# Optimization experiments

Hardware: AMD Instinct MI355X
Metric: run time of the kernel (lower is better)

## Reference

```python
import jax, jax.numpy as jnp
import numpy as np

H = 256   # hidden size
U = 10    # attention units


def _lstm_cell(xt, h, c, Wih, Whh, bih, bhh):
    # PyTorch gate order: i, f, g, o
    gates = xt @ Wih.T + h @ Whh.T + bih + bhh          # [B, 4H]
    i, f, g, o = jnp.split(gates, 4, axis=-1)
    i = jax.nn.sigmoid(i); f = jax.nn.sigmoid(f)
    g = jnp.tanh(g);       o = jax.nn.sigmoid(o)
    c = f * c + i * g
    h = o * jnp.tanh(c)
    return h, c


def setup_inputs() -> dict:
    key = jax.random.key(0)
    ks = jax.random.split(key, 12)
    B, S = 512, 256
    s = 1.0 / np.sqrt(H)
    x = jax.random.normal(ks[0], (B, S), dtype=jnp.float32)
    y = jax.random.randint(ks[1], (B, S), 0, S, dtype=jnp.int64)
    return {
        "x": x,
        "y": y,
        "enc_Wih": jax.random.uniform(ks[2], (4 * H, 1), jnp.float32, -s, s),
        "enc_Whh": jax.random.uniform(ks[3], (4 * H, H), jnp.float32, -s, s),
        "enc_bih": jax.random.uniform(ks[4], (4 * H,), jnp.float32, -s, s),
        "enc_bhh": jax.random.uniform(ks[5], (4 * H,), jnp.float32, -s, s),
        "dec_Wih": jax.random.uniform(ks[6], (4 * H, H + 1), jnp.float32, -s, s),
        "dec_Whh": jax.random.uniform(ks[7], (4 * H, H), jnp.float32, -s, s),
        "dec_bih": jax.random.uniform(ks[8], (4 * H,), jnp.float32, -s, s),
        "dec_bhh": jax.random.uniform(ks[9], (4 * H,), jnp.float32, -s, s),
        "att_W1": jax.random.uniform(ks[10], (U, H), jnp.float32, -s, s),
        "att_W2": jax.random.uniform(ks[11], (U, H), jnp.float32, -s, s),
        "att_V": jax.random.uniform(jax.random.fold_in(key, 99), (1, U), jnp.float32, -s, s),
    }


def reference(x, y, enc_Wih, enc_Whh, enc_bih, enc_bhh,
              dec_Wih, dec_Whh, dec_bih, dec_bhh,
              att_W1, att_W2, att_V):
    B, S = x.shape

    # ---- Encoder: LSTM over sequence of scalar inputs ----
    def enc_step(carry, xt):  # xt: [B, 1]
        h, c = carry
        h, c = _lstm_cell(xt, h, c, enc_Wih, enc_Whh, enc_bih, enc_bhh)
        return (h, c), h

    h0 = jnp.zeros((B, H), x.dtype)
    (hN, cN), enc_out_t = jax.lax.scan(enc_step, (h0, h0), x.T[:, :, None])
    enc_out = jnp.transpose(enc_out_t, (1, 0, 2))            # [B, S, H]

    # precompute W1 @ encoder_hidden (same math, hoisted out of loop)
    encW1 = jnp.einsum('bsh,uh->bsu', enc_out, att_W1)       # [B, S, U]

    # ---- Decoder loop (teacher forcing with ratio 1.0) ----
    def dec_step(carry, y_t):
        h, c, dec_in = carry                                  # dec_in: [B, 1]
        u = jnp.tanh(encW1 + (h @ att_W2.T)[:, None, :])      # [B, S, U]
        logits = jnp.einsum('bsu,ou->bso', u, att_V)[..., 0]  # [B, S]
        aj = jax.nn.softmax(logits, axis=1)
        di = jnp.einsum('bs,bsh->bh', aj, enc_out)            # [B, H]
        lstm_in = jnp.concatenate([di, dec_in], axis=1)       # [B, H+1]
        h, c = _lstm_cell(lstm_in, h, c, dec_Wih, dec_Whh, dec_bih, dec_bhh)
        pred = jnp.argmax(logits, axis=1)                     # [B]
        logp = jax.nn.log_softmax(logits, axis=1)
        loss_t = -jnp.mean(jnp.take_along_axis(logp, y_t[:, None], axis=1))
        dec_in_next = jnp.take_along_axis(x, y_t[:, None], axis=1)  # teacher force
        return (h, c, dec_in_next), (pred, loss_t)

    dec_in0 = jnp.zeros((B, 1), x.dtype)
    _, (preds, losses) = jax.lax.scan(dec_step, (hN, cN, dec_in0), y.T)
    outputs = preds[:, :, None].astype(jnp.int64)             # [S, B, 1]
    batch_loss = jnp.sum(losses) / B
    return outputs, batch_loss
```

## Files before the change

### kernel.cpp

```cpp
#include <hip/hip_runtime.h>
#include <cmath>

__device__ __forceinline__ double dexp_(double x) {
    x = fmin(fmax(x, -64.0), 64.0);
    double w = x * 1.4426950408889634;
    double n = rint(w);
    double u = (w - n) * 0.6931471805599453;
    double p = 1.0 + u * (1.0 + u * (0.5 + u * (1.6666666666666666e-01 +
               u * (4.1666666666666664e-02 + u * (8.3333333333333332e-03 +
               u * (1.3888888888888889e-03 + u * (1.9841269841269841e-04 +
               u * (2.4801587301587302e-05 + u * (2.7557319223985893e-06 +
               u * (2.7557319223985888e-07 + u * 2.5052108385441720e-08))))))))));
    return ldexp(p, (int)n);
}
__device__ __forceinline__ double dtanh_(double x) {
    double ax = fabs(x);
    double e = dexp_(2.0 * ax);
    double t = 1.0 - 2.0 / (e + 1.0);
    return copysign(t, x);
}
__device__ __forceinline__ double dsig_(double x) {
    return 1.0 / (1.0 + dexp_(-x));
}

__global__ __launch_bounds__(256) void prep_kernel(
    const float* __restrict__ eWih, const float* __restrict__ eWhh,
    const float* __restrict__ ebih, const float* __restrict__ ebhh,
    const float* __restrict__ dWih, const float* __restrict__ dWhh,
    const float* __restrict__ dbih, const float* __restrict__ dbhh,
    float* __restrict__ WencR, double* __restrict__ bencR,
    float* __restrict__ WdecR, double* __restrict__ bdecR)
{
    const int n_enc = 257 * 1024;
    const int n_dec = 513 * 1024;
    const int total = n_enc + n_dec + 2048;
    for (int idx = blockIdx.x * blockDim.x + threadIdx.x; idx < total;
         idx += gridDim.x * blockDim.x) {
        if (idx < n_enc) {
            int k = idx >> 10, c = idx & 1023;
            int j = c >> 2, g = c & 3, r = g * 256 + j;
            WencR[idx] = (k == 0) ? eWih[r] : eWhh[r * 256 + (k - 1)];
        } else if (idx < n_enc + n_dec) {
            int i2 = idx - n_enc;
            int k = i2 >> 10, c = i2 & 1023;
            int j = c >> 2, g = c & 3, r = g * 256 + j;
            WdecR[i2] = (k < 257) ? dWih[r * 257 + k] : dWhh[r * 256 + (k - 257)];
        } else {
            int c = idx - n_enc - n_dec;
            if (c < 1024) {
                int r = (c & 3) * 256 + (c >> 2);
                bencR[c] = (double)ebih[r] + (double)ebhh[r];
            } else {
                int c2 = c - 1024;
                int r = (c2 & 3) * 256 + (c2 >> 2);
                bdecR[c2] = (double)dbih[r] + (double)dbhh[r];
            }
        }
    }
}

__global__ __launch_bounds__(256) void lstm_enc_kernel(
    const float* __restrict__ x, const float* __restrict__ W,
    const double* __restrict__ bR, const float* __restrict__ h_in, long hin_str,
    float* __restrict__ h_out,
    float* __restrict__ c_st, int t)
{
    __shared__ float Xs[16 * 260];
    const int tid = threadIdx.x;
    const int row = tid & 15;
    const int jt  = tid >> 4;
    const int b0  = (blockIdx.x & 31) * 16;
    const int jg  = (blockIdx.x >> 5) * 16 + jt;

    #pragma unroll
    for (int i = 0; i < 4; ++i) {
        int idx = tid + i * 256;
        int r = idx >> 6;
        int c4 = (idx & 63) * 4;
        float4 v = *(const float4*)&h_in[(long)(b0 + r) * hin_str + c4];
        *(float4*)&Xs[r * 260 + c4] = v;
    }
    if (tid < 16) Xs[tid * 260 + 256] = x[(b0 + tid) * 256 + t];
    __syncthreads();

    const float* wp = W + jg * 4;
    double A0 = 0, A1 = 0, A2 = 0, A3 = 0;
    const float* xr = &Xs[row * 260];
    for (int k0 = 0; k0 < 256; k0 += 8) {
        float4 w[8];
        #pragma unroll
        for (int i = 0; i < 8; ++i)
            w[i] = *(const float4*)&wp[(1 + k0 + i) * 1024];
        float4 xa = *(const float4*)&xr[k0];
        float4 xb = *(const float4*)&xr[k0 + 4];
        float xs[8] = {xa.x, xa.y, xa.z, xa.w, xb.x, xb.y, xb.z, xb.w};
        float s0 = 0.f, s1 = 0.f, s2 = 0.f, s3 = 0.f;
        #pragma unroll
        for (int i = 0; i < 8; ++i) {
            s0 = fmaf(w[i].x, xs[i], s0);
            s1 = fmaf(w[i].y, xs[i], s1);
            s2 = fmaf(w[i].z, xs[i], s2);
            s3 = fmaf(w[i].w, xs[i], s3);
        }
        A0 += (double)s0; A1 += (double)s1;
        A2 += (double)s2; A3 += (double)s3;
    }
    {
        float4 w = *(const float4*)&wp[0];
        float xv = xr[256];
        A0 += (double)(w.x * xv); A1 += (double)(w.y * xv);
        A2 += (double)(w.z * xv); A3 += (double)(w.w * xv);
    }

    double bi = bR[jg * 4 + 0], bf = bR[jg * 4 + 1];
    double bg = bR[jg * 4 + 2], bo = bR[jg * 4 + 3];
    int b = b0 + row;
    double iv = dsig_(A0 + bi);
    double fv = dsig_(A1 + bf);
    double gv = dtanh_(A2 + bg);
    double ov = dsig_(A3 + bo);
    long ci = (long)b * 256 + jg;
    double c = fv * (double)c_st[ci] + iv * gv;
    c_st[ci] = (float)c;
    h_out[(long)b * 65536 + jg] = (float)(ov * dtanh_(c));
}

__global__ __launch_bounds__(256) void encW1_kernel(
    const float* __restrict__ enc_out, const float* __restrict__ W1,
    double* __restrict__ encW1d)
{
    __shared__ float sa[64][260];
    __shared__ float sw[10][257];
    const int tid = threadIdx.x;
    const int m0 = blockIdx.x * 64;
    #pragma unroll
    for (int i = 0; i < 16; ++i) {
        int idx = tid + i * 256;
        int row = idx >> 6;
        int c4 = (idx & 63) * 4;
        const float4 v = *(const float4*)&enc_out[(long)(m0 + row) * 256 + c4];
        *(float4*)&sa[row][c4] = v;
    }
    for (int i = tid; i < 2560; i += 256) sw[i >> 8][i & 255] = W1[i];
    __syncthreads();
    for (int o = tid; o < 640; o += 256) {
        int r = o / 10;
        int u = o - r * 10;
        double acc = 0.0;
        #pragma unroll 4
        for (int k = 0; k < 256; ++k)
            acc += (double)sa[r][k] * (double)sw[u][k];
        encW1d[(long)(m0 + r) * 10 + u] = acc;
    }
}

__global__ __launch_bounds__(256) void att_kernel(
    const double* __restrict__ encW1d, const float* __restrict__ enc_out,
    const float* __restrict__ W2, const float* __restrict__ V,
    const float* __restrict__ h_in, long hin_str, const int* __restrict__ y,
    float* __restrict__ di, float* __restrict__ logp_buf,
    float* __restrict__ out_pred, int t)
{
    const int b = blockIdx.x;
    const int s = threadIdx.x;
    const int wid = s >> 6, lane = s & 63;

    __shared__ float s_h[256];
    __shared__ double s_V[12];
    __shared__ double s_W2h[12];
    __shared__ double s_ld[256];
    __shared__ float s_e[256];
    __shared__ double s_red[4];
    __shared__ int s_redi[4];
    __shared__ double s_maxd, s_Zd;
    __shared__ int s_am;

    s_h[s] = h_in[(long)b * hin_str + s];
    if (s < 10) s_V[s] = (double)V[s];
    __syncthreads();

    for (int u = wid; u < 10; u += 4) {
        double p = 0.0;
        #pragma unroll
        for (int i = 0; i < 4; ++i) {
            int k = lane + i * 64;
            p += (double)W2[u * 256 + k] * (double)s_h[k];
        }
        #pragma unroll
        for (int off = 32; off >= 1; off >>= 1) p += __shfl_down(p, off, 64);
        if (lane == 0) s_W2h[u] = p;
    }
    __syncthreads();

    const double* eW = encW1d + ((long)b * 256 + s) * 10;
    double l = 0.0;
    #pragma unroll
    for (int u = 0; u < 10; ++u) l += s_V[u] * dtanh_(eW[u] + s_W2h[u]);
    s_ld[s] = l;

    {
        double v = l; int idx = s;
        #pragma unroll
        for (int off = 32; off >= 1; off >>= 1) {
            double v2 = __shfl_down(v, off, 64);
            int i2 = __shfl_down(idx, off, 64);
            if (v2 > v || (v2 == v && i2 < idx)) { v = v2; idx = i2; }
        }
        if (lane == 0) { s_red[wid] = v; s_redi[wid] = idx; }
    }
    __syncthreads();
    if (s == 0) {
        double v = s_red[0]; int idx = s_redi[0];
        #pragma unroll
        for (int w = 1; w < 4; ++w) {
            if (s_red[w] > v || (s_red[w] == v && s_redi[w] < idx)) {
                v = s_red[w]; idx = s_redi[w];
            }
        }
        s_maxd = v; s_am = idx;
    }
    __syncthreads();

    double e = dexp_(l - s_maxd);
    s_e[s] = (float)e;
    {
        double v = e;
        #pragma unroll
        for (int off = 32; off >= 1; off >>= 1) v += __shfl_down(v, off, 64);
        if (lane == 0) s_red[wid] = v;
    }
    __syncthreads();
    if (s == 0) {
        double Z = s_red[0] + s_red[1] + s_red[2] + s_red[3];
        s_Zd = Z;
        out_pred[t * 512 + b] = (float)s_am;
        int yv = y[b * 256 + t];
        logp_buf[t * 512 + b] = (float)(s_ld[yv] - s_maxd - log(Z));
    }
    __syncthreads();

    const float rcpZ = (float)(1.0 / s_Zd);
    const float* ep = enc_out + (long)b * 65536 + s;
    float acc0 = 0.f, acc1 = 0.f, acc2 = 0.f, acc3 = 0.f;
    for (int s2 = 0; s2 < 256; s2 += 4) {
        acc0 += s_e[s2 + 0] * ep[(s2 + 0) * 256];
        acc1 += s_e[s2 + 1] * ep[(s2 + 1) * 256];
        acc2 += s_e[s2 + 2] * ep[(s2 + 2) * 256];
        acc3 += s_e[s2 + 3] * ep[(s2 + 3) * 256];
    }
    di[b * 256 + s] = ((acc0 + acc1) + (acc2 + acc3)) * rcpZ;
}

__global__ __launch_bounds__(256) void lstm_dec_kernel(
    const float* __restrict__ x, const int* __restrict__ y,
    const float* __restrict__ W, const double* __restrict__ bR,
    const float* __restrict__ di, const float* __restrict__ h_in, long hin_str,
    float* __restrict__ h_out, float* __restrict__ c_st, int t)
{
    __shared__ float Xs[16 * 516];
    const int tid = threadIdx.x;
    const int row = tid & 15;
    const int jt  = tid >> 4;
    const int b0  = (blockIdx.x & 31) * 16;
    const int jg  = (blockIdx.x >> 5) * 16 + jt;

    #pragma unroll
    for (int i = 0; i < 4; ++i) {
        int idx = tid + i * 256;
        int r = idx >> 6;
        int c4 = (idx & 63) * 4;
        float4 v = *(const float4*)&di[(long)(b0 + r) * 256 + c4];
        *(float4*)&Xs[r * 516 + c4] = v;
        float4 u = *(const float4*)&h_in[(long)(b0 + r) * hin_str + c4];
        *(float4*)&Xs[r * 516 + 260 + c4] = u;
    }
    if (tid < 16) {
        int b = b0 + tid;
        float dv = 0.0f;
        if (t > 0) {
            int yi = y[b * 256 + (t - 1)];
            dv = x[b * 256 + yi];
        }
        Xs[tid * 516 + 256] = dv;
    }
    __syncthreads();

    const float* wp = W + jg * 4;
    double A0 = 0, A1 = 0, A2 = 0, A3 = 0;
    const float* xr = &Xs[row * 516];

    for (int k0 = 0; k0 < 256; k0 += 8) {
        float4 w[8];
        #pragma unroll
        for (int i = 0; i < 8; ++i)
            w[i] = *(const float4*)&wp[(k0 + i) * 1024];
        float4 xa = *(const float4*)&xr[k0];
        float4 xb = *(const float4*)&xr[k0 + 4];
        float xs[8] = {xa.x, xa.y, xa.z, xa.w, xb.x, xb.y, xb.z, xb.w};
        float s0 = 0.f, s1 = 0.f, s2 = 0.f, s3 = 0.f;
        #pragma unroll
        for (int i = 0; i < 8; ++i) {
            s0 = fmaf(w[i].x, xs[i], s0);
            s1 = fmaf(w[i].y, xs[i], s1);
            s2 = fmaf(w[i].z, xs[i], s2);
            s3 = fmaf(w[i].w, xs[i], s3);
        }
        A0 += (double)s0; A1 += (double)s1;
        A2 += (double)s2; A3 += (double)s3;
    }
    {
        float4 w = *(const float4*)&wp[256 * 1024];
        float xv = xr[256];
        A0 += (double)(w.x * xv); A1 += (double)(w.y * xv);
        A2 += (double)(w.z * xv); A3 += (double)(w.w * xv);
    }
    for (int k0 = 0; k0 < 256; k0 += 8) {
        float4 w[8];
        #pragma unroll
        for (int i = 0; i < 8; ++i)
            w[i] = *(const float4*)&wp[(257 + k0 + i) * 1024];
        float4 xa = *(const float4*)&xr[260 + k0];
        float4 xb = *(const float4*)&xr[260 + k0 + 4];
        float xs[8] = {xa.x, xa.y, xa.z, xa.w, xb.x, xb.y, xb.z, xb.w};
        float s0 = 0.f, s1 = 0.f, s2 = 0.f, s3 = 0.f;
        #pragma unroll
        for (int i = 0; i < 8; ++i) {
            s0 = fmaf(w[i].x, xs[i], s0);
            s1 = fmaf(w[i].y, xs[i], s1);
            s2 = fmaf(w[i].z, xs[i], s2);
            s3 = fmaf(w[i].w, xs[i], s3);
        }
        A0 += (double)s0; A1 += (double)s1;
        A2 += (double)s2; A3 += (double)s3;
    }

    double bi = bR[jg * 4 + 0], bf = bR[jg * 4 + 1];
    double bg = bR[jg * 4 + 2], bo = bR[jg * 4 + 3];
    int b = b0 + row;
    double iv = dsig_(A0 + bi);
    double fv = dsig_(A1 + bf);
    double gv = dtanh_(A2 + bg);
    double ov = dsig_(A3 + bo);
    long ci = (long)b * 256 + jg;
    double c = fv * (double)c_st[ci] + iv * gv;
    c_st[ci] = (float)c;
    h_out[ci] = (float)(ov * dtanh_(c));
}

__global__ __launch_bounds__(256) void loss_kernel(
    const float* __restrict__ logp_buf, float* __restrict__ out)
{
    const int tid = threadIdx.x;
    double acc = 0.0;
    for (int i = tid; i < 131072; i += 256) acc += (double)logp_buf[i];
    __shared__ double s_red[4];
    const int wid = tid >> 6, lane = tid & 63;
    #pragma unroll
    for (int off = 32; off >= 1; off >>= 1) acc += __shfl_down(acc, off, 64);
    if (lane == 0) s_red[wid] = acc;
    __syncthreads();
    if (tid == 0) {
        out[131072] = (float)(-(s_red[0] + s_red[1] + s_red[2] + s_red[3])
                              / (512.0 * 512.0));
    }
}

extern "C" void kernel_launch(void* const* d_in, const int* in_sizes, int n_in,
                              void* d_out, int out_size, void* d_ws, size_t ws_size,
                              hipStream_t stream)
{
    const float* x    = (const float*)d_in[0];
    const int*   y    = (const int*)  d_in[1];
    const float* eWih = (const float*)d_in[2];
    const float* eWhh = (const float*)d_in[3];
    const float* ebih = (const float*)d_in[4];
    const float* ebhh = (const float*)d_in[5];
    const float* dWih = (const float*)d_in[6];
    const float* dWhh = (const float*)d_in[7];
    const float* dbih = (const float*)d_in[8];
    const float* dbhh = (const float*)d_in[9];
    const float* W1   = (const float*)d_in[10];
    const float* W2   = (const float*)d_in[11];
    const float* V    = (const float*)d_in[12];

    double* encW1d = (double*)d_ws;
    double* bencR  = encW1d + 1310720;
    double* bdecR  = bencR + 1024;
    float* enc_out = (float*)(bdecR + 1024);
    float* c_st    = enc_out + 33554432;
    float* hzero   = c_st + 131072;
    float* hd      = hzero + 131072;
    float* dibuf   = hd + 262144;
    float* logp    = dibuf + 131072;
    float* WencR   = logp + 131072;
    float* WdecR   = WencR + 263168;

    float* out = (float*)d_out;

    hipMemsetAsync(c_st, 0, 131072 * sizeof(float), stream);
    hipMemsetAsync(hzero, 0, 131072 * sizeof(float), stream);

    prep_kernel<<<512, 256, 0, stream>>>(eWih, eWhh, ebih, ebhh,
                                         dWih, dWhh, dbih, dbhh,
                                         WencR, bencR, WdecR, bdecR);

    for (int t = 0; t < 256; ++t) {
        const float* hin; long hstr;
        if (t == 0) { hin = hzero; hstr = 256; }
        else        { hin = enc_out + (long)(t - 1) * 256; hstr = 65536; }
        lstm_enc_kernel<<<512, 256, 0, stream>>>(x, WencR, bencR, hin, hstr,
                                                 enc_out + (long)t * 256, c_st, t);
    }

    encW1_kernel<<<2048, 256, 0, stream>>>(enc_out, W1, encW1d);

    for (int t = 0; t < 256; ++t) {
        const float* hin; long hstr;
        if (t == 0) { hin = enc_out + 255 * 256; hstr = 65536; }
        else        { hin = hd + (t & 1) * 131072; hstr = 256; }
        float* hout = hd + ((t + 1) & 1) * 131072;
        att_kernel<<<512, 256, 0, stream>>>(encW1d, enc_out, W2, V, hin, hstr,
                                            y, dibuf, logp, out, t);
        lstm_dec_kernel<<<512, 256, 0, stream>>>(x, y, WdecR, bdecR, dibuf,
                                                 hin, hstr, hout, c_st, t);
    }

    loss_kernel<<<1, 256, 0, stream>>>(logp, out);
}
```

Measured before the change: 19.73 ms.

## Tile LSTM weight layout per block, swap thread mapping, and software-prefetch loads

Repacks the encoder and decoder LSTM weights so that each 16-column tile used by one block occupies a contiguous chunk. The thread mapping is swapped so that adjacent lanes read adjacent float4 weights, which makes weight loads coalesced, while the hidden-state row is read from shared memory with a broadcast pattern. Weight loads in the gate matmuls and enc_out loads in the attention context sum are double-buffered in registers so the next chunk's global loads overlap the current FMAs. This raises register pressure and changes the shared-memory access pattern across lanes.

```diff
diff --git a/kernel.cpp b/kernel.cpp
--- a/kernel.cpp
+++ b/kernel.cpp
@@ -37,13 +37,17 @@
     for (int idx = blockIdx.x * blockDim.x + threadIdx.x; idx < total;
          idx += gridDim.x * blockDim.x) {
         if (idx < n_enc) {
-            int k = idx >> 10, c = idx & 1023;
-            int j = c >> 2, g = c & 3, r = g * 256 + j;
+            int tile = idx / 16448;
+            int rem  = idx - tile * 16448;
+            int k = rem >> 6, c = rem & 63;
+            int j = tile * 16 + (c >> 2), g = c & 3, r = g * 256 + j;
             WencR[idx] = (k == 0) ? eWih[r] : eWhh[r * 256 + (k - 1)];
         } else if (idx < n_enc + n_dec) {
             int i2 = idx - n_enc;
-            int k = i2 >> 10, c = i2 & 1023;
-            int j = c >> 2, g = c & 3, r = g * 256 + j;
+            int tile = i2 / 32832;
+            int rem  = i2 - tile * 32832;
+            int k = rem >> 6, c = rem & 63;
+            int j = tile * 16 + (c >> 2), g = c & 3, r = g * 256 + j;
             WdecR[i2] = (k < 257) ? dWih[r * 257 + k] : dWhh[r * 256 + (k - 257)];
         } else {
             int c = idx - n_enc - n_dec;
@@ -67,10 +71,11 @@
 {
     __shared__ float Xs[16 * 260];
     const int tid = threadIdx.x;
-    const int row = tid & 15;
-    const int jt  = tid >> 4;
+    const int jt  = tid & 15;
+    const int row = tid >> 4;
     const int b0  = (blockIdx.x & 31) * 16;
-    const int jg  = (blockIdx.x >> 5) * 16 + jt;
+    const int JT  = blockIdx.x >> 5;
+    const int jg  = JT * 16 + jt;
 
     #pragma unroll
     for (int i = 0; i < 4; ++i) {
@@ -83,30 +88,36 @@
     if (tid < 16) Xs[tid * 260 + 256] = x[(b0 + tid) * 256 + t];
     __syncthreads();
 
-    const float* wp = W + jg * 4;
+    const float4* wp4 = (const float4*)(W + (size_t)JT * 16448) + jt;
+    const float* xr = &Xs[row * 260];
     double A0 = 0, A1 = 0, A2 = 0, A3 = 0;
-    const float* xr = &Xs[row * 260];
+
+    float4 wa[8];
+    #pragma unroll
+    for (int i = 0; i < 8; ++i) wa[i] = wp4[(1 + i) * 16];
     for (int k0 = 0; k0 < 256; k0 += 8) {
-        float4 w[8];
-        #pragma unroll
-        for (int i = 0; i < 8; ++i)
-            w[i] = *(const float4*)&wp[(1 + k0 + i) * 1024];
+        int kn = (k0 + 8) & 255;
+        float4 wb[8];
+        #pragma unroll
+        for (int i = 0; i < 8; ++i) wb[i] = wp4[(1 + kn + i) * 16];
         float4 xa = *(const float4*)&xr[k0];
         float4 xb = *(const float4*)&xr[k0 + 4];
         float xs[8] = {xa.x, xa.y, xa.z, xa.w, xb.x, xb.y, xb.z, xb.w};
-        float s0 = 0.f, s1 = 0.f, s2 = 0.f, s3 = 0.f;
+        float p0 = 0.f, p1 = 0.f, p2 = 0.f, p3 = 0.f;
         #pragma unroll
         for (int i = 0; i < 8; ++i) {
-            s0 = fmaf(w[i].x, xs[i], s0);
-            s1 = fmaf(w[i].y, xs[i], s1);
-            s2 = fmaf(w[i].z, xs[i], s2);
-            s3 = fmaf(w[i].w, xs[i], s3);
-        }
-        A0 += (double)s0; A1 += (double)s1;
-        A2 += (double)s2; A3 += (double)s3;
+            p0 = fmaf(wa[i].x, xs[i], p0);
+            p1 = fmaf(wa[i].y, xs[i], p1);
+            p2 = fmaf(wa[i].z, xs[i], p2);
+            p3 = fmaf(wa[i].w, xs[i], p3);
+        }
+        A0 += (double)p0; A1 += (double)p1;
+        A2 += (double)p2; A3 += (double)p3;
+        #pragma unroll
+        for (int i = 0; i < 8; ++i) wa[i] = wb[i];
     }
     {
-        float4 w = *(const float4*)&wp[0];
+        float4 w = wp4[0];
         float xv = xr[256];
         A0 += (double)(w.x * xv); A1 += (double)(w.y * xv);
         A2 += (double)(w.z * xv); A3 += (double)(w.w * xv);
@@ -241,14 +252,23 @@
 
     const float rcpZ = (float)(1.0 / s_Zd);
     const float* ep = enc_out + (long)b * 65536 + s;
-    float acc0 = 0.f, acc1 = 0.f, acc2 = 0.f, acc3 = 0.f;
-    for (int s2 = 0; s2 < 256; s2 += 4) {
-        acc0 += s_e[s2 + 0] * ep[(s2 + 0) * 256];
-        acc1 += s_e[s2 + 1] * ep[(s2 + 1) * 256];
-        acc2 += s_e[s2 + 2] * ep[(s2 + 2) * 256];
-        acc3 += s_e[s2 + 3] * ep[(s2 + 3) * 256];
-    }
-    di[b * 256 + s] = ((acc0 + acc1) + (acc2 + acc3)) * rcpZ;
+    float acc[8] = {0.f,0.f,0.f,0.f,0.f,0.f,0.f,0.f};
+    float v[8];
+    #pragma unroll
+    for (int i = 0; i < 8; ++i) v[i] = ep[i * 256];
+    for (int s2 = 0; s2 < 256; s2 += 8) {
+        int sn = (s2 + 8) & 255;
+        float vn[8];
+        #pragma unroll
+        for (int i = 0; i < 8; ++i) vn[i] = ep[(sn + i) * 256];
+        #pragma unroll
+        for (int i = 0; i < 8; ++i) acc[i] = fmaf(s_e[s2 + i], v[i], acc[i]);
+        #pragma unroll
+        for (int i = 0; i < 8; ++i) v[i] = vn[i];
+    }
+    float r01 = acc[0] + acc[1], r23 = acc[2] + acc[3];
+    float r45 = acc[4] + acc[5], r67 = acc[6] + acc[7];
+    di[b * 256 + s] = ((r01 + r23) + (r45 + r67)) * rcpZ;
 }
 
 __global__ __launch_bounds__(256) void lstm_dec_kernel(
@@ -259,10 +279,11 @@
 {
     __shared__ float Xs[16 * 516];
     const int tid = threadIdx.x;
-    const int row = tid & 15;
-    const int jt  = tid >> 4;
+    const int jt  = tid & 15;
+    const int row = tid >> 4;
     const int b0  = (blockIdx.x & 31) * 16;
-    const int jg  = (blockIdx.x >> 5) * 16 + jt;
+    const int JT  = blockIdx.x >> 5;
+    const int jg  = JT * 16 + jt;
 
     #pragma unroll
     for (int i = 0; i < 4; ++i) {
@@ -285,53 +306,62 @@
     }
     __syncthreads();
 
-    const float* wp = W + jg * 4;
+    const float4* wp4 = (const float4*)(W + (size_t)JT * 32832) + jt;
+    const float* xr = &Xs[row * 516];
     double A0 = 0, A1 = 0, A2 = 0, A3 = 0;
-    const float* xr = &Xs[row * 516];
-
+
+    float4 wa[8];
+    #pragma unroll
+    for (int i = 0; i < 8; ++i) wa[i] = wp4[i * 16];
     for (int k0 = 0; k0 < 256; k0 += 8) {
-        float4 w[8];
-        #pragma unroll
-        for (int i = 0; i < 8; ++i)
-            w[i] = *(const float4*)&wp[(k0 + i) * 1024];
+        int kn = (k0 + 8) & 255;
+        float4 wb[8];
+        #pragma unroll
+        for (int i = 0; i < 8; ++i) wb[i] = wp4[(kn + i) * 16];
         float4 xa = *(const float4*)&xr[k0];
         float4 xb = *(const float4*)&xr[k0 + 4];
         float xs[8] = {xa.x, xa.y, xa.z, xa.w, xb.x, xb.y, xb.z, xb.w};
-        float s0 = 0.f, s1 = 0.f, s2 = 0.f, s3 = 0.f;
+        float p0 = 0.f, p1 = 0.f, p2 = 0.f, p3 = 0.f;
         #pragma unroll
         for (int i = 0; i < 8; ++i) {
-            s0 = fmaf(w[i].x, xs[i], s0);
-            s1 = fmaf(w[i].y, xs[i], s1);
-            s2 = fmaf(w[i].z, xs[i], s2);
-            s3 = fmaf(w[i].w, xs[i], s3);
-        }
-        A0 += (double)s0; A1 += (double)s1;
-        A2 += (double)s2; A3 += (double)s3;
+            p0 = fmaf(wa[i].x, xs[i], p0);
+            p1 = fmaf(wa[i].y, xs[i], p1);
+            p2 = fmaf(wa[i].z, xs[i], p2);
+            p3 = fmaf(wa[i].w, xs[i], p3);
+        }
+        A0 += (double)p0; A1 += (double)p1;
+        A2 += (double)p2; A3 += (double)p3;
+        #pragma unroll
+        for (int i = 0; i < 8; ++i) wa[i] = wb[i];
     }
     {
-        float4 w = *(const float4*)&wp[256 * 1024];
+        float4 w = wp4[256 * 16];
         float xv = xr[256];
         A0 += (double)(w.x * xv); A1 += (double)(w.y * xv);
         A2 += (double)(w.z * xv); A3 += (double)(w.w * xv);
     }
+    #pragma unroll
+    for (int i = 0; i < 8; ++i) wa[i] = wp4[(257 + i) * 16];
     for (int k0 = 0; k0 < 256; k0 += 8) {
-        float4 w[8];
-        #pragma unroll
-        for (int i = 0; i < 8; ++i)
-            w[i] = *(const float4*)&wp[(257 + k0 + i) * 1024];
+        int kn = (k0 + 8) & 255;
+        float4 wb[8];
+        #pragma unroll
+        for (int i = 0; i < 8; ++i) wb[i] = wp4[(257 + kn + i) * 16];
         float4 xa = *(const float4*)&xr[260 + k0];
         float4 xb = *(const float4*)&xr[260 + k0 + 4];
         float xs[8] = {xa.x, xa.y, xa.z, xa.w, xb.x, xb.y, xb.z, xb.w};
-        float s0 = 0.f, s1 = 0.f, s2 = 0.f, s3 = 0.f;
+        float p0 = 0.f, p1 = 0.f, p2 = 0.f, p3 = 0.f;
         #pragma unroll
         for (int i = 0; i < 8; ++i) {
-            s0 = fmaf(w[i].x, xs[i], s0);
-            s1 = fmaf(w[i].y, xs[i], s1);
-            s2 = fmaf(w[i].z, xs[i], s2);
-            s3 = fmaf(w[i].w, xs[i], s3);
-        }
-        A0 += (double)s0; A1 += (double)s1;
-        A2 += (double)s2; A3 += (double)s3;
+            p0 = fmaf(wa[i].x, xs[i], p0);
+            p1 = fmaf(wa[i].y, xs[i], p1);
+            p2 = fmaf(wa[i].z, xs[i], p2);
+            p3 = fmaf(wa[i].w, xs[i], p3);
+        }
+        A0 += (double)p0; A1 += (double)p1;
+        A2 += (double)p2; A3 += (double)p3;
+        #pragma unroll
+        for (int i = 0; i < 8; ++i) wa[i] = wb[i];
     }
 
     double bi = bR[jg * 4 + 0], bf = bR[jg * 4 + 1];
```

Measured after the change: 44.30 ms. 2.25x slower.

## Fuse encoder, attention and decoder loops into one persistent kernel per batch pair

Applied to the files above, without the earlier changes.

Replaces the 768 per-timestep launches (encoder LSTM, encW1, attention, decoder LSTM) with a single persistent kernel where each 512-thread block owns two batch rows and iterates over all timesteps. Hidden and cell state stay in shared memory and registers, so the h/c/di global round-trips and launch overhead go away. The cost is that each block re-reads the full recurrent weight matrices from L2 every timestep for only two batch rows, so weight reuse across batch is lost. With only 256 blocks the GPU may also be underoccupied.

```diff
diff --git a/kernel.cpp b/kernel.cpp
--- a/kernel.cpp
+++ b/kernel.cpp
@@ -59,292 +59,260 @@
     }
 }
 
-__global__ __launch_bounds__(256) void lstm_enc_kernel(
-    const float* __restrict__ x, const float* __restrict__ W,
-    const double* __restrict__ bR, const float* __restrict__ h_in, long hin_str,
-    float* __restrict__ h_out,
-    float* __restrict__ c_st, int t)
+__global__ __launch_bounds__(512) void persist_kernel(
+    const float* __restrict__ x, const int* __restrict__ y,
+    const float* __restrict__ W1, const float* __restrict__ W2,
+    const float* __restrict__ V,
+    const float* __restrict__ WencR, const double* __restrict__ bencR,
+    const float* __restrict__ WdecR, const double* __restrict__ bdecR,
+    float* __restrict__ enc_out, double* __restrict__ encW1d,
+    float* __restrict__ logp, float* __restrict__ out)
 {
-    __shared__ float Xs[16 * 260];
     const int tid = threadIdx.x;
-    const int row = tid & 15;
-    const int jt  = tid >> 4;
-    const int b0  = (blockIdx.x & 31) * 16;
-    const int jg  = (blockIdx.x >> 5) * 16 + jt;
-
-    #pragma unroll
-    for (int i = 0; i < 4; ++i) {
-        int idx = tid + i * 256;
-        int r = idx >> 6;
-        int c4 = (idx & 63) * 4;
-        float4 v = *(const float4*)&h_in[(long)(b0 + r) * hin_str + c4];
-        *(float4*)&Xs[r * 260 + c4] = v;
-    }
-    if (tid < 16) Xs[tid * 260 + 256] = x[(b0 + tid) * 256 + t];
+    const int bid = blockIdx.x;
+    const int b   = tid >> 8;
+    const int j   = tid & 255;
+    const int ab  = bid * 2 + b;
+    const int hwid = (tid >> 6) & 3;
+    const int lane = tid & 63;
+
+    __shared__ float Xs[2][516];
+    __shared__ double s_V[12];
+    __shared__ double s_W2h[2][12];
+    __shared__ double s_ld[2][256];
+    __shared__ float s_e[2][256];
+    __shared__ double s_red[2][4];
+    __shared__ int s_redi[2][4];
+    __shared__ double s_maxd[2], s_Zd[2];
+    __shared__ int s_am[2];
+
+    Xs[b][260 + j] = 0.0f;
+    if (tid < 10) s_V[tid] = (double)V[tid];
+    float c_reg = 0.0f;
     __syncthreads();
 
-    const float* wp = W + jg * 4;
-    double A0 = 0, A1 = 0, A2 = 0, A3 = 0;
-    const float* xr = &Xs[row * 260];
-    for (int k0 = 0; k0 < 256; k0 += 8) {
-        float4 w[8];
-        #pragma unroll
-        for (int i = 0; i < 8; ++i)
-            w[i] = *(const float4*)&wp[(1 + k0 + i) * 1024];
-        float4 xa = *(const float4*)&xr[k0];
-        float4 xb = *(const float4*)&xr[k0 + 4];
-        float xs[8] = {xa.x, xa.y, xa.z, xa.w, xb.x, xb.y, xb.z, xb.w};
-        float s0 = 0.f, s1 = 0.f, s2 = 0.f, s3 = 0.f;
-        #pragma unroll
-        for (int i = 0; i < 8; ++i) {
-            s0 = fmaf(w[i].x, xs[i], s0);
-            s1 = fmaf(w[i].y, xs[i], s1);
-            s2 = fmaf(w[i].z, xs[i], s2);
-            s3 = fmaf(w[i].w, xs[i], s3);
+    {
+        const float* wp = WencR + j * 4;
+        const double bi = bencR[j*4+0], bf = bencR[j*4+1];
+        const double bg = bencR[j*4+2], bo = bencR[j*4+3];
+        for (int t = 0; t < 256; ++t) {
+            if (tid < 2) Xs[tid][257] = x[(bid * 2 + tid) * 256 + t];
+            __syncthreads();
+
+            double A0 = 0, A1 = 0, A2 = 0, A3 = 0;
+            const float* xr = &Xs[b][260];
+            for (int k0 = 0; k0 < 256; k0 += 8) {
+                float4 w[8];
+                #pragma unroll
+                for (int i = 0; i < 8; ++i)
+                    w[i] = *(const float4*)&wp[(1 + k0 + i) * 1024];
+                float4 xa = *(const float4*)&xr[k0];
+                float4 xb = *(const float4*)&xr[k0 + 4];
+                float xs[8] = {xa.x, xa.y, xa.z, xa.w, xb.x, xb.y, xb.z, xb.w};
+                float p0 = 0.f, p1 = 0.f, p2 = 0.f, p3 = 0.f;
+                #pragma unroll
+                for (int i = 0; i < 8; ++i) {
+                    p0 = fmaf(w[i].x, xs[i], p0);
+                    p1 = fmaf(w[i].y, xs[i], p1);
+                    p2 = fmaf(w[i].z, xs[i], p2);
+                    p3 = fmaf(w[i].w, xs[i], p3);
+                }
+                A0 += (double)p0; A1 += (double)p1;
+                A2 += (double)p2; A3 += (double)p3;
+            }
+            {
+                float4 w = *(const float4*)&wp[0];
+                float xv = Xs[b][257];
+                A0 += (double)(w.x * xv); A1 += (double)(w.y * xv);
+                A2 += (double)(w.z * xv); A3 += (double)(w.w * xv);
+            }
+            double iv = dsig_(A0 + bi);
+            double fv = dsig_(A1 + bf);
+            double gv = dtanh_(A2 + bg);
+            double ov = dsig_(A3 + bo);
+            double c = fv * (double)c_reg + iv * gv;
+            c_reg = (float)c;
+            float hn = (float)(ov * dtanh_(c));
+            __syncthreads();
+            Xs[b][260 + j] = hn;
+            enc_out[(long)ab * 65536 + t * 256 + j] = hn;
         }
-        A0 += (double)s0; A1 += (double)s1;
-        A2 += (double)s2; A3 += (double)s3;
-    }
+    }
+    __syncthreads();
+    __threadfence_block();
+
     {
-        float4 w = *(const float4*)&wp[0];
-        float xv = xr[256];
-        A0 += (double)(w.x * xv); A1 += (double)(w.y * xv);
-        A2 += (double)(w.z * xv); A3 += (double)(w.w * xv);
-    }
-
-    double bi = bR[jg * 4 + 0], bf = bR[jg * 4 + 1];
-    double bg = bR[jg * 4 + 2], bo = bR[jg * 4 + 3];
-    int b = b0 + row;
-    double iv = dsig_(A0 + bi);
-    double fv = dsig_(A1 + bf);
-    double gv = dtanh_(A2 + bg);
-    double ov = dsig_(A3 + bo);
-    long ci = (long)b * 256 + jg;
-    double c = fv * (double)c_st[ci] + iv * gv;
-    c_st[ci] = (float)c;
-    h_out[(long)b * 65536 + jg] = (float)(ov * dtanh_(c));
-}
-
-__global__ __launch_bounds__(256) void encW1_kernel(
-    const float* __restrict__ enc_out, const float* __restrict__ W1,
-    double* __restrict__ encW1d)
-{
-    __shared__ float sa[64][260];
-    __shared__ float sw[10][257];
-    const int tid = threadIdx.x;
-    const int m0 = blockIdx.x * 64;
-    #pragma unroll
-    for (int i = 0; i < 16; ++i) {
-        int idx = tid + i * 256;
-        int row = idx >> 6;
-        int c4 = (idx & 63) * 4;
-        const float4 v = *(const float4*)&enc_out[(long)(m0 + row) * 256 + c4];
-        *(float4*)&sa[row][c4] = v;
-    }
-    for (int i = tid; i < 2560; i += 256) sw[i >> 8][i & 255] = W1[i];
-    __syncthreads();
-    for (int o = tid; o < 640; o += 256) {
-        int r = o / 10;
-        int u = o - r * 10;
-        double acc = 0.0;
-        #pragma unroll 4
-        for (int k = 0; k < 256; ++k)
-            acc += (double)sa[r][k] * (double)sw[u][k];
-        encW1d[(long)(m0 + r) * 10 + u] = acc;
-    }
-}
-
-__global__ __launch_bounds__(256) void att_kernel(
-    const double* __restrict__ encW1d, const float* __restrict__ enc_out,
-    const float* __restrict__ W2, const float* __restrict__ V,
-    const float* __restrict__ h_in, long hin_str, const int* __restrict__ y,
-    float* __restrict__ di, float* __restrict__ logp_buf,
-    float* __restrict__ out_pred, int t)
-{
-    const int b = blockIdx.x;
-    const int s = threadIdx.x;
-    const int wid = s >> 6, lane = s & 63;
-
-    __shared__ float s_h[256];
-    __shared__ double s_V[12];
-    __shared__ double s_W2h[12];
-    __shared__ double s_ld[256];
-    __shared__ float s_e[256];
-    __shared__ double s_red[4];
-    __shared__ int s_redi[4];
-    __shared__ double s_maxd, s_Zd;
-    __shared__ int s_am;
-
-    s_h[s] = h_in[(long)b * hin_str + s];
-    if (s < 10) s_V[s] = (double)V[s];
-    __syncthreads();
-
-    for (int u = wid; u < 10; u += 4) {
-        double p = 0.0;
-        #pragma unroll
-        for (int i = 0; i < 4; ++i) {
-            int k = lane + i * 64;
-            p += (double)W2[u * 256 + k] * (double)s_h[k];
+        const long m = (long)bid * 512 + tid;
+        const float* er = enc_out + m * 256;
+        double acc[10] = {0,0,0,0,0,0,0,0,0,0};
+        for (int k = 0; k < 256; ++k) {
+            double ev = (double)er[k];
+            #pragma unroll
+            for (int u = 0; u < 10; ++u)
+                acc[u] += ev * (double)W1[u * 256 + k];
         }
         #pragma unroll
-        for (int off = 32; off >= 1; off >>= 1) p += __shfl_down(p, off, 64);
-        if (lane == 0) s_W2h[u] = p;
+        for (int u = 0; u < 10; ++u) encW1d[m * 10 + u] = acc[u];
     }
     __syncthreads();
 
-    const double* eW = encW1d + ((long)b * 256 + s) * 10;
-    double l = 0.0;
-    #pragma unroll
-    for (int u = 0; u < 10; ++u) l += s_V[u] * dtanh_(eW[u] + s_W2h[u]);
-    s_ld[s] = l;
-
     {
-        double v = l; int idx = s;
-        #pragma unroll
-        for (int off = 32; off >= 1; off >>= 1) {
-            double v2 = __shfl_down(v, off, 64);
-            int i2 = __shfl_down(idx, off, 64);
-            if (v2 > v || (v2 == v && i2 < idx)) { v = v2; idx = i2; }
+        const float* dwp = WdecR + j * 4;
+        const double bi = bdecR[j*4+0], bf = bdecR[j*4+1];
+        const double bg = bdecR[j*4+2], bo = bdecR[j*4+3];
+        const int s = j;
+
+        for (int t = 0; t < 256; ++t) {
+            __syncthreads();
+
+            for (int u = hwid; u < 10; u += 4) {
+                double p = 0.0;
+                #pragma unroll
+                for (int i = 0; i < 4; ++i) {
+                    int k = lane + i * 64;
+                    p += (double)W2[u * 256 + k] * (double)Xs[b][260 + k];
+                }
+                #pragma unroll
+                for (int off = 32; off >= 1; off >>= 1) p += __shfl_down(p, off, 64);
+                if (lane == 0) s_W2h[b][u] = p;
+            }
+            __syncthreads();
+
+            const double* eW = encW1d + ((long)ab * 256 + s) * 10;
+            double l = 0.0;
+            #pragma unroll
+            for (int u = 0; u < 10; ++u)
+                l += s_V[u] * dtanh_(eW[u] + s_W2h[b][u]);
+            s_ld[b][s] = l;
+            {
+                double v = l; int idx = s;
+                #pragma unroll
+                for (int off = 32; off >= 1; off >>= 1) {
+                    double v2 = __shfl_down(v, off, 64);
+                    int i2 = __shfl_down(idx, off, 64);
+                    if (v2 > v || (v2 == v && i2 < idx)) { v = v2; idx = i2; }
+                }
+                if (lane == 0) { s_red[b][hwid] = v; s_redi[b][hwid] = idx; }
+            }
+            __syncthreads();
+            if (s == 0) {
+                double v = s_red[b][0]; int idx = s_redi[b][0];
+                #pragma unroll
+                for (int w = 1; w < 4; ++w) {
+                    if (s_red[b][w] > v || (s_red[b][w] == v && s_redi[b][w] < idx)) {
+                        v = s_red[b][w]; idx = s_redi[b][w];
+                    }
+                }
+                s_maxd[b] = v; s_am[b] = idx;
+            }
+            __syncthreads();
+
+            double e = dexp_(l - s_maxd[b]);
+            s_e[b][s] = (float)e;
+            {
+                double v = e;
+                #pragma unroll
+                for (int off = 32; off >= 1; off >>= 1) v += __shfl_down(v, off, 64);
+                if (lane == 0) s_red[b][hwid] = v;
+            }
+            __syncthreads();
+            if (s == 0) {
+                double Z = s_red[b][0] + s_red[b][1] + s_red[b][2] + s_red[b][3];
+                s_Zd[b] = Z;
+                out[t * 512 + ab] = (float)s_am[b];
+                int yv = y[ab * 256 + t];
+                logp[t * 512 + ab] = (float)(s_ld[b][yv] - s_maxd[b] - log(Z));
+                float dv = 0.0f;
+                if (t > 0) {
+                    int yi = y[ab * 256 + (t - 1)];
+                    dv = x[ab * 256 + yi];
+                }
+                Xs[b][256] = dv;
+            }
+            __syncthreads();
+
+            {
+                const float rcpZ = (float)(1.0 / s_Zd[b]);
+                const float* ep = enc_out + (long)ab * 65536 + s;
+                float acc[8] = {0.f,0.f,0.f,0.f,0.f,0.f,0.f,0.f};
+                float v[8];
+                #pragma unroll
+                for (int i = 0; i < 8; ++i) v[i] = ep[i * 256];
+                for (int s2 = 0; s2 < 256; s2 += 8) {
+                    int sn = (s2 + 8) & 255;
+                    float vn[8];
+                    #pragma unroll
+                    for (int i = 0; i < 8; ++i) vn[i] = ep[(sn + i) * 256];
+                    #pragma unroll
+                    for (int i = 0; i < 8; ++i)
+                        acc[i] = fmaf(s_e[b][s2 + i], v[i], acc[i]);
+                    #pragma unroll
+                    for (int i = 0; i < 8; ++i) v[i] = vn[i];
+                }
+                float r01 = acc[0] + acc[1], r23 = acc[2] + acc[3];
+                float r45 = acc[4] + acc[5], r67 = acc[6] + acc[7];
+                Xs[b][s] = ((r01 + r23) + (r45 + r67)) * rcpZ;
+            }
+            __syncthreads();
+
+            double A0 = 0, A1 = 0, A2 = 0, A3 = 0;
+            const float* xr = &Xs[b][0];
+            for (int k0 = 0; k0 < 256; k0 += 8) {
+                float4 w[8];
+                #pragma unroll
+                for (int i = 0; i < 8; ++i)
+                    w[i] = *(const float4*)&dwp[(k0 + i) * 1024];
+                float4 xa = *(const float4*)&xr[k0];
+                float4 xb = *(const float4*)&xr[k0 + 4];
+                float xs[8] = {xa.x, xa.y, xa.z, xa.w, xb.x, xb.y, xb.z, xb.w};
+                float p0 = 0.f, p1 = 0.f, p2 = 0.f, p3 = 0.f;
+                #pragma unroll
+                for (int i = 0; i < 8; ++i) {
+                    p0 = fmaf(w[i].x, xs[i], p0);
+                    p1 = fmaf(w[i].y, xs[i], p1);
+                    p2 = fmaf(w[i].z, xs[i], p2);
+                    p3 = fmaf(w[i].w, xs[i], p3);
+                }
+                A0 += (double)p0; A1 += (double)p1;
+                A2 += (double)p2; A3 += (double)p3;
+            }
+            {
+                float4 w = *(const float4*)&dwp[256 * 1024];
+                float xv = xr[256];
+                A0 += (double)(w.x * xv); A1 += (double)(w.y * xv);
+                A2 += (double)(w.z * xv); A3 += (double)(w.w * xv);
+            }
+            for (int k0 = 0; k0 < 256; k0 += 8) {
+                float4 w[8];
+                #pragma unroll
+                for (int i = 0; i < 8; ++i)
+                    w[i] = *(const float4*)&dwp[(257 + k0 + i) * 1024];
+                float4 xa = *(const float4*)&xr[260 + k0];
+                float4 xb = *(const float4*)&xr[260 + k0 + 4];
+                float xs[8] = {xa.x, xa.y, xa.z, xa.w, xb.x, xb.y, xb.z, xb.w};
+                float p0 = 0.f, p1 = 0.f, p2 = 0.f, p3 = 0.f;
+                #pragma unroll
+                for (int i = 0; i < 8; ++i) {
+                    p0 = fmaf(w[i].x, xs[i], p0);
+                    p1 = fmaf(w[i].y, xs[i], p1);
+                    p2 = fmaf(w[i].z, xs[i], p2);
+                    p3 = fmaf(w[i].w, xs[i], p3);
+                }
+                A0 += (double)p0; A1 += (double)p1;
+                A2 += (double)p2; A3 += (double)p3;
+            }
+
+            double iv = dsig_(A0 + bi);
+            double fv = dsig_(A1 + bf);
+            double gv = dtanh_(A2 + bg);
+            double ov = dsig_(A3 + bo);
+            double c = fv * (double)c_reg + iv * gv;
+            c_reg = (float)c;
+            float hn = (float)(ov * dtanh_(c));
+            __syncthreads();
+            Xs[b][260 + j] = hn;
         }
-        if (lane == 0) { s_red[wid] = v; s_redi[wid] = idx; }
-    }
-    __syncthreads();
-    if (s == 0) {
-        double v = s_red[0]; int idx = s_redi[0];
-        #pragma unroll
-        for (int w = 1; w < 4; ++w) {
-            if (s_red[w] > v || (s_red[w] == v && s_redi[w] < idx)) {
-                v = s_red[w]; idx = s_redi[w];
-            }
-        }
-        s_maxd = v; s_am = idx;
-    }
-    __syncthreads();
-
-    double e = dexp_(l - s_maxd);
-    s_e[s] = (float)e;
-    {
-        double v = e;
-        #pragma unroll
-        for (int off = 32; off >= 1; off >>= 1) v += __shfl_down(v, off, 64);
-        if (lane == 0) s_red[wid] = v;
-    }
-    __syncthreads();
-    if (s == 0) {
-        double Z = s_red[0] + s_red[1] + s_red[2] + s_red[3];
-        s_Zd = Z;
-        out_pred[t * 512 + b] = (float)s_am;
-        int yv = y[b * 256 + t];
-        logp_buf[t * 512 + b] = (float)(s_ld[yv] - s_maxd - log(Z));
-    }
-    __syncthreads();
-
-    const float rcpZ = (float)(1.0 / s_Zd);
-    const float* ep = enc_out + (long)b * 65536 + s;
-    float acc0 = 0.f, acc1 = 0.f, acc2 = 0.f, acc3 = 0.f;
-    for (int s2 = 0; s2 < 256; s2 += 4) {
-        acc0 += s_e[s2 + 0] * ep[(s2 + 0) * 256];
-        acc1 += s_e[s2 + 1] * ep[(s2 + 1) * 256];
-        acc2 += s_e[s2 + 2] * ep[(s2 + 2) * 256];
-        acc3 += s_e[s2 + 3] * ep[(s2 + 3) * 256];
-    }
-    di[b * 256 + s] = ((acc0 + acc1) + (acc2 + acc3)) * rcpZ;
-}
-
-__global__ __launch_bounds__(256) void lstm_dec_kernel(
-    const float* __restrict__ x, const int* __restrict__ y,
-    const float* __restrict__ W, const double* __restrict__ bR,
-    const float* __restrict__ di, const float* __restrict__ h_in, long hin_str,
-    float* __restrict__ h_out, float* __restrict__ c_st, int t)
-{
-    __shared__ float Xs[16 * 516];
-    const int tid = threadIdx.x;
-    const int row = tid & 15;
-    const int jt  = tid >> 4;
-    const int b0  = (blockIdx.x & 31) * 16;
-    const int jg  = (blockIdx.x >> 5) * 16 + jt;
-
-    #pragma unroll
-    for (int i = 0; i < 4; ++i) {
-        int idx = tid + i * 256;
-        int r = idx >> 6;
-        int c4 = (idx & 63) * 4;
-        float4 v = *(const float4*)&di[(long)(b0 + r) * 256 + c4];
-        *(float4*)&Xs[r * 516 + c4] = v;
-        float4 u = *(const float4*)&h_in[(long)(b0 + r) * hin_str + c4];
-        *(float4*)&Xs[r * 516 + 260 + c4] = u;
-    }
-    if (tid < 16) {
-        int b = b0 + tid;
-        float dv = 0.0f;
-        if (t > 0) {
-            int yi = y[b * 256 + (t - 1)];
-            dv = x[b * 256 + yi];
-        }
-        Xs[tid * 516 + 256] = dv;
-    }
-    __syncthreads();
-
-    const float* wp = W + jg * 4;
-    double A0 = 0, A1 = 0, A2 = 0, A3 = 0;
-    const float* xr = &Xs[row * 516];
-
-    for (int k0 = 0; k0 < 256; k0 += 8) {
-        float4 w[8];
-        #pragma unroll
-        for (int i = 0; i < 8; ++i)
-            w[i] = *(const float4*)&wp[(k0 + i) * 1024];
-        float4 xa = *(const float4*)&xr[k0];
-        float4 xb = *(const float4*)&xr[k0 + 4];
-        float xs[8] = {xa.x, xa.y, xa.z, xa.w, xb.x, xb.y, xb.z, xb.w};
-        float s0 = 0.f, s1 = 0.f, s2 = 0.f, s3 = 0.f;
-        #pragma unroll
-        for (int i = 0; i < 8; ++i) {
-            s0 = fmaf(w[i].x, xs[i], s0);
-            s1 = fmaf(w[i].y, xs[i], s1);
-            s2 = fmaf(w[i].z, xs[i], s2);
-            s3 = fmaf(w[i].w, xs[i], s3);
-        }
-        A0 += (double)s0; A1 += (double)s1;
-        A2 += (double)s2; A3 += (double)s3;
-    }
-    {
-        float4 w = *(const float4*)&wp[256 * 1024];
-        float xv = xr[256];
-        A0 += (double)(w.x * xv); A1 += (double)(w.y * xv);
-        A2 += (double)(w.z * xv); A3 += (double)(w.w * xv);
-    }
-    for (int k0 = 0; k0 < 256; k0 += 8) {
-        float4 w[8];
-        #pragma unroll
-        for (int i = 0; i < 8; ++i)
-            w[i] = *(const float4*)&wp[(257 + k0 + i) * 1024];
-        float4 xa = *(const float4*)&xr[260 + k0];
-        float4 xb = *(const float4*)&xr[260 + k0 + 4];
-        float xs[8] = {xa.x, xa.y, xa.z, xa.w, xb.x, xb.y, xb.z, xb.w};
-        float s0 = 0.f, s1 = 0.f, s2 = 0.f, s3 = 0.f;
-        #pragma unroll
-        for (int i = 0; i < 8; ++i) {
-            s0 = fmaf(w[i].x, xs[i], s0);
-            s1 = fmaf(w[i].y, xs[i], s1);
-            s2 = fmaf(w[i].z, xs[i], s2);
-            s3 = fmaf(w[i].w, xs[i], s3);
-        }
-        A0 += (double)s0; A1 += (double)s1;
-        A2 += (double)s2; A3 += (double)s3;
-    }
-
-    double bi = bR[jg * 4 + 0], bf = bR[jg * 4 + 1];
-    double bg = bR[jg * 4 + 2], bo = bR[jg * 4 + 3];
-    int b = b0 + row;
-    double iv = dsig_(A0 + bi);
-    double fv = dsig_(A1 + bf);
-    double gv = dtanh_(A2 + bg);
-    double ov = dsig_(A3 + bo);
-    long ci = (long)b * 256 + jg;
-    double c = fv * (double)c_st[ci] + iv * gv;
-    c_st[ci] = (float)c;
-    h_out[ci] = (float)(ov * dtanh_(c));
+    }
 }
 
 __global__ __launch_bounds__(256) void loss_kernel(
@@ -387,43 +355,19 @@
     double* bencR  = encW1d + 1310720;
     double* bdecR  = bencR + 1024;
     float* enc_out = (float*)(bdecR + 1024);
-    float* c_st    = enc_out + 33554432;
-    float* hzero   = c_st + 131072;
-    float* hd      = hzero + 131072;
-    float* dibuf   = hd + 262144;
-    float* logp    = dibuf + 131072;
+    float* logp    = enc_out + 33554432;
     float* WencR   = logp + 131072;
     float* WdecR   = WencR + 263168;
 
     float* out = (float*)d_out;
-
-    hipMemsetAsync(c_st, 0, 131072 * sizeof(float), stream);
-    hipMemsetAsync(hzero, 0, 131072 * sizeof(float), stream);
 
     prep_kernel<<<512, 256, 0, stream>>>(eWih, eWhh, ebih, ebhh,
                                          dWih, dWhh, dbih, dbhh,
                                          WencR, bencR, WdecR, bdecR);
 
-    for (int t = 0; t < 256; ++t) {
-        const float* hin; long hstr;
-        if (t == 0) { hin = hzero; hstr = 256; }
-        else        { hin = enc_out + (long)(t - 1) * 256; hstr = 65536; }
-        lstm_enc_kernel<<<512, 256, 0, stream>>>(x, WencR, bencR, hin, hstr,
-                                                 enc_out + (long)t * 256, c_st, t);
-    }
-
-    encW1_kernel<<<2048, 256, 0, stream>>>(enc_out, W1, encW1d);
-
-    for (int t = 0; t < 256; ++t) {
-        const float* hin; long hstr;
-        if (t == 0) { hin = enc_out + 255 * 256; hstr = 65536; }
-        else        { hin = hd + (t & 1) * 131072; hstr = 256; }
-        float* hout = hd + ((t + 1) & 1) * 131072;
-        att_kernel<<<512, 256, 0, stream>>>(encW1d, enc_out, W2, V, hin, hstr,
-                                            y, dibuf, logp, out, t);
-        lstm_dec_kernel<<<512, 256, 0, stream>>>(x, y, WdecR, bdecR, dibuf,
-                                                 hin, hstr, hout, c_st, t);
-    }
+    persist_kernel<<<256, 512, 0, stream>>>(x, y, W1, W2, V,
+                                            WencR, bencR, WdecR, bdecR,
+                                            enc_out, encW1d, logp, out);
 
     loss_kernel<<<1, 256, 0, stream>>>(logp, out);
 }
```

Measured after the change: 55.58 ms. 2.82x slower.
